# Kernel optimization log

Hardware: AMD Instinct MI355X
Metric: run time of the kernel (lower is better)

Reference implementation:

```python
import jax, jax.numpy as jnp
import numpy as np

ALPHA = 0.2  # LeakyReLU negative slope


def setup_inputs() -> dict:
    key = jax.random.key(0)
    k1, k2, k3, k4 = jax.random.split(key, 4)
    bs, L, D, F_in, F_out = 8, 4096, 16, 128, 128
    x = jax.random.normal(k1, (bs, L, F_in), dtype=jnp.float32)
    adj = jax.random.randint(k2, (bs, L, D), 0, L, dtype=jnp.int64)
    # xavier_normal-ish init for params
    W = jax.random.normal(k3, (F_in, F_out), dtype=jnp.float32) * (1.414 * (2.0 / (F_in + F_out)) ** 0.5)
    a = jax.random.normal(k4, (2 * F_out, 1), dtype=jnp.float32) * (1.414 * (2.0 / (2 * F_out + 1)) ** 0.5)
    return {"x": x, "adj": adj, "W": W, "a": a}


def reference(x, adj, W, a):
    # x: [B, L, F_in], adj: [B, L, D] int node indices, W: [F_in, F_out], a: [2*F_out, 1]
    # Project first, then gather (same math as gather-then-project, fewer FLOPs).
    h = jnp.matmul(x, W)                                  # [B, L, F_out]
    h_prime = jax.vmap(lambda hb, ab: hb[ab])(h, adj)     # [B, L, D, F_out]
    # h_node: neighbor-0 features broadcast over D (torch repeat_interleave of h_prime[:,:,0:1,:])
    h_node = jnp.broadcast_to(h_prime[:, :, :1, :], h_prime.shape)
    # attention logits: concat(h_prime, h_node) @ a -> [B, L, D, 1]
    e = jnp.concatenate([h_prime, h_node], axis=-1) @ a
    e = jnp.where(e > 0, e, ALPHA * e)                    # LeakyReLU
    attn = jax.nn.softmax(e[..., 0], axis=-1)             # softmax over neighbors D -> [B, L, D]
    # dropout is identity in eval mode (p=0.0)
    out = jnp.einsum('bld,bldf->blf', attn, h_prime)      # weighted aggregate -> [B, L, F_out]
    return jax.nn.elu(out)                                # concat=True branch
```

## Files before the change

### kernel.cpp

```cpp
#include <hip/hip_runtime.h>
#include <hip/hip_bf16.h>

#define BATCH 8
#define SEQ   4096
#define DEG   16
#define FD    128
#define NTOT  (BATCH * SEQ)
#define ALPHA 0.2f
#define LDS_WK 132

typedef __attribute__((ext_vector_type(8))) short short8v;
typedef __attribute__((ext_vector_type(4))) short short4v;
typedef __attribute__((ext_vector_type(4))) float float4v;
typedef __attribute__((ext_vector_type(4))) float f32x4;
typedef __attribute__((ext_vector_type(2))) float f32x2;

__device__ __forceinline__ unsigned short f2bf(float f) {
    unsigned int u = __float_as_uint(f);
    u += 0x7fffu + ((u >> 16) & 1u);
    return (unsigned short)(u >> 16);
}

__global__ __launch_bounds__(256) void gat_proj(
    const float* __restrict__ x, const float* __restrict__ W,
    const float* __restrict__ avec, unsigned short* __restrict__ hb,
    float2* __restrict__ s12)
{
    __shared__ unsigned short Wt[128 * LDS_WK];

    const int t = threadIdx.x;
    const int bid = blockIdx.x;
    const int xcd = bid & 7, blk = bid >> 3;
    const long long rowBase = (long long)xcd * SEQ + (long long)blk * 64;

    {
        const int q = t & 31;
        const int kh = t >> 5;
        #pragma unroll
        for (int j = 0; j < 8; ++j) {
            const int kp = kh + 8 * j;
            const f32x4 w0 = *reinterpret_cast<const f32x4*>(&W[(2 * kp) * FD + 4 * q]);
            const f32x4 w1 = *reinterpret_cast<const f32x4*>(&W[(2 * kp + 1) * FD + 4 * q]);
            #pragma unroll
            for (int e2 = 0; e2 < 4; ++e2) {
                const unsigned int pk = (unsigned int)f2bf(w0[e2])
                                      | ((unsigned int)f2bf(w1[e2]) << 16);
                *reinterpret_cast<unsigned int*>(&Wt[(4 * q + e2) * LDS_WK + 2 * kp]) = pk;
            }
        }
    }

    const int lane = t & 63, wv = t >> 6;
    const int g = lane >> 4, mrow = lane & 15;
    const long long node = rowBase + wv * 16 + mrow;
    short8v xfrag[4];
    {
        const float* xr = x + node * FD + 4 * g;
        #pragma unroll
        for (int kb = 0; kb < 4; ++kb) {
            const f32x4 x0 = __builtin_nontemporal_load(
                reinterpret_cast<const f32x4*>(xr + 32 * kb));
            const f32x4 x1 = __builtin_nontemporal_load(
                reinterpret_cast<const f32x4*>(xr + 32 * kb + 16));
            short8v f;
            f[0] = (short)f2bf(x0[0]); f[1] = (short)f2bf(x0[1]);
            f[2] = (short)f2bf(x0[2]); f[3] = (short)f2bf(x0[3]);
            f[4] = (short)f2bf(x1[0]); f[5] = (short)f2bf(x1[1]);
            f[6] = (short)f2bf(x1[2]); f[7] = (short)f2bf(x1[3]);
            xfrag[kb] = f;
        }
    }
    __syncthreads();

    float4v acc[8];
    #pragma unroll
    for (int tn = 0; tn < 8; ++tn) { acc[tn][0] = 0.f; acc[tn][1] = 0.f; acc[tn][2] = 0.f; acc[tn][3] = 0.f; }

    #pragma unroll
    for (int tn = 0; tn < 8; ++tn) {
        const int nbase = (16 * tn + mrow) * LDS_WK + 4 * g;
        #pragma unroll
        for (int kb = 0; kb < 4; ++kb) {
            const short4v lo = *reinterpret_cast<const short4v*>(&Wt[nbase + 32 * kb]);
            const short4v hi = *reinterpret_cast<const short4v*>(&Wt[nbase + 32 * kb + 16]);
            short8v wf;
            wf[0] = lo[0]; wf[1] = lo[1]; wf[2] = lo[2]; wf[3] = lo[3];
            wf[4] = hi[0]; wf[5] = hi[1]; wf[6] = hi[2]; wf[7] = hi[3];
            acc[tn] = __builtin_amdgcn_mfma_f32_16x16x32_bf16(wf, xfrag[kb], acc[tn], 0, 0, 0);
        }
    }

    float s1p = 0.f, s2p = 0.f;
    #pragma unroll
    for (int tn = 0; tn < 8; ++tn) {
        const int col = 16 * tn + 4 * g;
        const unsigned int u0 = (unsigned int)f2bf(acc[tn][0])
                              | ((unsigned int)f2bf(acc[tn][1]) << 16);
        const unsigned int u1 = (unsigned int)f2bf(acc[tn][2])
                              | ((unsigned int)f2bf(acc[tn][3]) << 16);
        *reinterpret_cast<uint2*>(&hb[node * FD + col]) = make_uint2(u0, u1);
        const f32x4 a1 = *reinterpret_cast<const f32x4*>(&avec[col]);
        const f32x4 a2 = *reinterpret_cast<const f32x4*>(&avec[FD + col]);
        #pragma unroll
        for (int r = 0; r < 4; ++r) {
            s1p = fmaf(acc[tn][r], a1[r], s1p);
            s2p = fmaf(acc[tn][r], a2[r], s2p);
        }
    }
    s1p += __shfl_xor(s1p, 16, 64);  s2p += __shfl_xor(s2p, 16, 64);
    s1p += __shfl_xor(s1p, 32, 64);  s2p += __shfl_xor(s2p, 32, 64);
    if (lane < 16)
        s12[rowBase + wv * 16 + lane] = make_float2(s1p, s2p);
}

__global__ __launch_bounds__(256) void gat_aggr(
    const int* __restrict__ adj, const unsigned short* __restrict__ hb,
    const float2* __restrict__ s12, float* __restrict__ out)
{
    const int t = threadIdx.x;
    const int lane = t & 63;
    const int wv_u = __builtin_amdgcn_readfirstlane(t) >> 6;
    const int bid = blockIdx.x;
    const int xcd = bid & 7, blk = bid >> 3;
    const int node = xcd * SEQ + blk * 4 + wv_u;
    const int bBase = xcd * SEQ;

    const int* ap = adj + node * DEG;
    int nb[16];
    #pragma unroll
    for (int d = 0; d < 16; ++d) nb[d] = ap[d];

    const int c = lane & 15;
    const int nbc = ap[c];
    const float s2n0 = s12[bBase + nb[0]].y;
    float ev = s12[bBase + nbc].x + s2n0;
    ev = ev > 0.f ? ev : ALPHA * ev;
    float p = __expf(ev);
    float sum = p;
    #pragma unroll
    for (int mo = 1; mo < 16; mo <<= 1) sum += __shfl_xor(sum, mo, 64);
    p *= 1.f / sum;

    float a0 = 0.f, a1 = 0.f;
    #pragma unroll
    for (int d = 0; d < 16; ++d) {
        const float pd = __uint_as_float(
            __builtin_amdgcn_readlane(__float_as_uint(p), d));
        const unsigned int* rp = reinterpret_cast<const unsigned int*>(
            hb + (((long long)(bBase + nb[d])) << 7));
        const unsigned int u = rp[lane];
        a0 = fmaf(pd, __uint_as_float(u << 16), a0);
        a1 = fmaf(pd, __uint_as_float(u & 0xffff0000u), a1);
    }

    f32x2 o;
    o[0] = a0 > 0.f ? a0 : (__expf(a0) - 1.f);
    o[1] = a1 > 0.f ? a1 : (__expf(a1) - 1.f);
    __builtin_nontemporal_store(o, reinterpret_cast<f32x2*>(
        out + (long long)node * FD + lane * 2));
}

extern "C" void kernel_launch(void* const* d_in, const int* in_sizes, int n_in,
                              void* d_out, int out_size, void* d_ws, size_t ws_size,
                              hipStream_t stream) {
    const float* x  = (const float*)d_in[0];
    const int* adj  = (const int*)d_in[1];
    const float* W  = (const float*)d_in[2];
    const float* a  = (const float*)d_in[3];
    float* out = (float*)d_out;

    unsigned short* hb = (unsigned short*)d_ws;
    float2* s12 = (float2*)((char*)d_ws + (size_t)NTOT * FD * 2);

    gat_proj<<<dim3(NTOT / 64), dim3(256), 0, stream>>>(x, W, a, hb, s12);
    gat_aggr<<<dim3(NTOT / 4), dim3(256), 0, stream>>>(adj, hb, s12, out);
}
```

Before: 23.01 us.

## Fuse projection and aggregation into one cooperative kernel with grid sync

Merges the projection and neighbor-aggregation kernels into a single cooperative launch of 512 blocks separated by a grid-wide barrier. Each wave then aggregates 16 nodes in a loop instead of one node per wave. The aim is to remove the second kernel launch and its inter-kernel gap. In exchange it adds grid-sync overhead and runs the gather phase with far fewer waves in flight, which may reduce latency hiding on the random hb gathers.

```diff
diff --git a/kernel.cpp b/kernel.cpp
--- a/kernel.cpp
+++ b/kernel.cpp
@@ -1,5 +1,8 @@
 #include <hip/hip_runtime.h>
 #include <hip/hip_bf16.h>
+#include <hip/hip_cooperative_groups.h>
+
+namespace cg = cooperative_groups;
 
 #define BATCH 8
 #define SEQ   4096
@@ -21,17 +24,20 @@
     return (unsigned short)(u >> 16);
 }
 
-__global__ __launch_bounds__(256) void gat_proj(
+__global__ __launch_bounds__(256, 2) void gat_fused(
     const float* __restrict__ x, const float* __restrict__ W,
-    const float* __restrict__ avec, unsigned short* __restrict__ hb,
-    float2* __restrict__ s12)
+    const float* __restrict__ avec, const int* __restrict__ adj,
+    unsigned short* __restrict__ hb, float2* __restrict__ s12,
+    float* __restrict__ out)
 {
     __shared__ unsigned short Wt[128 * LDS_WK];
 
     const int t = threadIdx.x;
     const int bid = blockIdx.x;
     const int xcd = bid & 7, blk = bid >> 3;
-    const long long rowBase = (long long)xcd * SEQ + (long long)blk * 64;
+    const int bBase = xcd * SEQ;
+    const long long rowBase = (long long)bBase + (long long)blk * 64;
+
 
     {
         const int q = t & 31;
@@ -52,10 +58,10 @@
 
     const int lane = t & 63, wv = t >> 6;
     const int g = lane >> 4, mrow = lane & 15;
-    const long long node = rowBase + wv * 16 + mrow;
+    const long long node1 = rowBase + wv * 16 + mrow;
     short8v xfrag[4];
     {
-        const float* xr = x + node * FD + 4 * g;
+        const float* xr = x + node1 * FD + 4 * g;
         #pragma unroll
         for (int kb = 0; kb < 4; ++kb) {
             const f32x4 x0 = __builtin_nontemporal_load(
@@ -98,7 +104,7 @@
                               | ((unsigned int)f2bf(acc[tn][1]) << 16);
         const unsigned int u1 = (unsigned int)f2bf(acc[tn][2])
                               | ((unsigned int)f2bf(acc[tn][3]) << 16);
-        *reinterpret_cast<uint2*>(&hb[node * FD + col]) = make_uint2(u0, u1);
+        *reinterpret_cast<uint2*>(&hb[node1 * FD + col]) = make_uint2(u0, u1);
         const f32x4 a1 = *reinterpret_cast<const f32x4*>(&avec[col]);
         const f32x4 a2 = *reinterpret_cast<const f32x4*>(&avec[FD + col]);
         #pragma unroll
@@ -111,53 +117,48 @@
     s1p += __shfl_xor(s1p, 32, 64);  s2p += __shfl_xor(s2p, 32, 64);
     if (lane < 16)
         s12[rowBase + wv * 16 + lane] = make_float2(s1p, s2p);
-}
 
-__global__ __launch_bounds__(256) void gat_aggr(
-    const int* __restrict__ adj, const unsigned short* __restrict__ hb,
-    const float2* __restrict__ s12, float* __restrict__ out)
-{
-    const int t = threadIdx.x;
-    const int lane = t & 63;
+    cg::this_grid().sync();
+
     const int wv_u = __builtin_amdgcn_readfirstlane(t) >> 6;
-    const int bid = blockIdx.x;
-    const int xcd = bid & 7, blk = bid >> 3;
-    const int node = xcd * SEQ + blk * 4 + wv_u;
-    const int bBase = xcd * SEQ;
+    const int c = lane & 15;
+    const int nodeBase = bBase + blk * 64 + wv_u * 16;
 
-    const int* ap = adj + node * DEG;
-    int nb[16];
-    #pragma unroll
-    for (int d = 0; d < 16; ++d) nb[d] = ap[d];
+    for (int j = 0; j < 16; ++j) {
+        const int node = nodeBase + j;
+        const int* ap = adj + (long long)node * DEG;
+        int nb[16];
+        #pragma unroll
+        for (int d = 0; d < 16; ++d) nb[d] = ap[d];
 
-    const int c = lane & 15;
-    const int nbc = ap[c];
-    const float s2n0 = s12[bBase + nb[0]].y;
-    float ev = s12[bBase + nbc].x + s2n0;
-    ev = ev > 0.f ? ev : ALPHA * ev;
-    float p = __expf(ev);
-    float sum = p;
-    #pragma unroll
-    for (int mo = 1; mo < 16; mo <<= 1) sum += __shfl_xor(sum, mo, 64);
-    p *= 1.f / sum;
+        const int nbc = ap[c];
+        const float s2n0 = s12[bBase + nb[0]].y;
+        float ev = s12[bBase + nbc].x + s2n0;
+        ev = ev > 0.f ? ev : ALPHA * ev;
+        float p = __expf(ev);
+        float sum = p;
+        #pragma unroll
+        for (int mo = 1; mo < 16; mo <<= 1) sum += __shfl_xor(sum, mo, 64);
+        p *= 1.f / sum;
 
-    float a0 = 0.f, a1 = 0.f;
-    #pragma unroll
-    for (int d = 0; d < 16; ++d) {
-        const float pd = __uint_as_float(
-            __builtin_amdgcn_readlane(__float_as_uint(p), d));
-        const unsigned int* rp = reinterpret_cast<const unsigned int*>(
-            hb + (((long long)(bBase + nb[d])) << 7));
-        const unsigned int u = rp[lane];
-        a0 = fmaf(pd, __uint_as_float(u << 16), a0);
-        a1 = fmaf(pd, __uint_as_float(u & 0xffff0000u), a1);
+        float a0 = 0.f, a1 = 0.f;
+        #pragma unroll
+        for (int d = 0; d < 16; ++d) {
+            const float pd = __uint_as_float(
+                __builtin_amdgcn_readlane(__float_as_uint(p), d));
+            const unsigned int* rp = reinterpret_cast<const unsigned int*>(
+                hb + (((long long)(bBase + nb[d])) << 7));
+            const unsigned int u = rp[lane];
+            a0 = fmaf(pd, __uint_as_float(u << 16), a0);
+            a1 = fmaf(pd, __uint_as_float(u & 0xffff0000u), a1);
+        }
+
+        f32x2 o;
+        o[0] = a0 > 0.f ? a0 : (__expf(a0) - 1.f);
+        o[1] = a1 > 0.f ? a1 : (__expf(a1) - 1.f);
+        __builtin_nontemporal_store(o, reinterpret_cast<f32x2*>(
+            out + (long long)node * FD + lane * 2));
     }
-
-    f32x2 o;
-    o[0] = a0 > 0.f ? a0 : (__expf(a0) - 1.f);
-    o[1] = a1 > 0.f ? a1 : (__expf(a1) - 1.f);
-    __builtin_nontemporal_store(o, reinterpret_cast<f32x2*>(
-        out + (long long)node * FD + lane * 2));
 }
 
 extern "C" void kernel_launch(void* const* d_in, const int* in_sizes, int n_in,
@@ -172,6 +173,8 @@
     unsigned short* hb = (unsigned short*)d_ws;
     float2* s12 = (float2*)((char*)d_ws + (size_t)NTOT * FD * 2);
 
-    gat_proj<<<dim3(NTOT / 64), dim3(256), 0, stream>>>(x, W, a, hb, s12);
-    gat_aggr<<<dim3(NTOT / 4), dim3(256), 0, stream>>>(adj, hb, s12, out);
+    void* args[] = {(void*)&x, (void*)&W, (void*)&a, (void*)&adj,
+                    (void*)&hb, (void*)&s12, (void*)&out};
+    hipLaunchCooperativeKernel((const void*)gat_fused, dim3(512), dim3(256),
+                               args, 0, stream);
 }
```

Result: slower. 86.02 us (+273.9%).
